# Kernel optimization log

Hardware: AMD Instinct MI355X
Metric: run time of the kernel (lower is better)

The kernel has to match this reference:

```python
import jax, jax.numpy as jnp
import numpy as np

B, T, D, H = 4, 1024, 1024, 16
TP = 1024
HD = D // H
LN_EPS = 1e-3  # keras LayerNormalization default epsilon


def snac_linear(x, wt, mt):
    # conv1dsnac: w = tanh(wt) * sigmoid(mt), shape [1, nx, nf] -> [nx, nf]
    w = (jnp.tanh(wt) * jax.nn.sigmoid(mt))[0]
    return jnp.einsum('btx,xf->btf', x, w)


def layernorm(x, gamma, beta):
    mu = jnp.mean(x, axis=-1, keepdims=True)
    var = jnp.mean(jnp.square(x - mu), axis=-1, keepdims=True)
    return (x - mu) * jax.lax.rsqrt(var + LN_EPS) * gamma + beta


def setup_inputs() -> dict:
    key = jax.random.key(0)
    ks = jax.random.split(key, 10)
    s = 0.02
    return {
        'input': jax.random.normal(ks[0], (B, T, D), jnp.float32),
        'past': jax.random.normal(ks[1], (B, 2, H, TP, HD), jnp.float32),
        'qkv_wt': jax.random.normal(ks[2], (1, D, 3 * D), jnp.float32) * s,
        'qkv_mt': jax.random.normal(ks[3], (1, D, 3 * D), jnp.float32) * s,
        'merge_wt': jax.random.normal(ks[4], (1, D, D), jnp.float32) * s,
        'merge_mt': jax.random.normal(ks[5], (1, D, D), jnp.float32) * s,
        'ln1_wt': jax.random.normal(ks[6], (1, D, D), jnp.float32) * s,
        'ln1_mt': jax.random.normal(ks[7], (1, D, D), jnp.float32) * s,
        'g1': jnp.ones((D,), jnp.float32), 'b1': jnp.zeros((D,), jnp.float32),
        'g2': jnp.ones((D,), jnp.float32), 'b2': jnp.zeros((D,), jnp.float32),
    }


def reference(input, past, qkv_wt, qkv_mt, merge_wt, merge_mt, ln1_wt, ln1_mt, g1, b1, g2, b2):
    x = input
    xn = layernorm(x, g1, b1)
    c = snac_linear(xn, qkv_wt, qkv_mt)  # [B, T, 3D]
    q, k, v = jnp.split(c, 3, axis=2)
    # split heads -> [B, H, T, HD]
    to_heads = lambda t: t.reshape(B, T, H, HD).transpose(0, 2, 1, 3)
    q, k, v = to_heads(q), to_heads(k), to_heads(v)
    present = jnp.stack([k, v], axis=1)  # [B, 2, H, T, HD]
    pk, pv = past[:, 0], past[:, 1]
    k = jnp.concatenate([pk, k], axis=2)  # [B, H, TP+T, HD]
    v = jnp.concatenate([pv, v], axis=2)
    nd, ns = T, TP + T
    w = jnp.einsum('bhqd,bhkd->bhqk', q, k) * jax.lax.rsqrt(jnp.float32(HD))
    i = jnp.arange(nd)[:, None]
    j = jnp.arange(ns)[None, :]
    m = (i >= j - ns + nd).astype(w.dtype)  # [nd, ns] causal mask incl. past
    w = w * m - jnp.asarray(1e10, w.dtype) * (1 - m)
    msk = jax.nn.softmax(w, axis=-1)  # [B, H, T, TP+T]
    a = jnp.einsum('bhqk,bhkd->bhqd', msk, v)
    ah = a.transpose(0, 2, 1, 3).reshape(B, T, D)  # merge heads
    am = snac_linear(ah, merge_wt, merge_mt)
    xa = x + am
    mlp = snac_linear(layernorm(xa, g2, b2), ln1_wt, ln1_mt)
    xm = xa + mlp
    return xm, present, msk
```

## Files before the change

kernel.cpp:

```cpp
#include <hip/hip_runtime.h>
#include <hip/hip_bf16.h>

typedef _Float16 half8 __attribute__((ext_vector_type(8)));
typedef _Float16 half4v __attribute__((ext_vector_type(4)));
typedef float f32x4 __attribute__((ext_vector_type(4)));

#define DEV static __device__ __forceinline__


typedef __attribute__((address_space(1))) const unsigned int* gas_p;
typedef __attribute__((address_space(3))) unsigned int* las_p;
DEV void glds16(const void* g, void* s) {
  __builtin_amdgcn_global_load_lds((gas_p)g, (las_p)s, 16, 0, 0);
}

__global__ __launch_bounds__(256) void prep_all(const float* __restrict__ qkv_wt,
                                                const float* __restrict__ qkv_mt,
                                                const float* __restrict__ mg_wt,
                                                const float* __restrict__ mg_mt,
                                                const float* __restrict__ l1_wt,
                                                const float* __restrict__ l1_mt,
                                                _Float16* __restrict__ wq,
                                                _Float16* __restrict__ wm,
                                                _Float16* __restrict__ wl) {
  __shared__ float tile[64][65];
  const float *wt, *mt;
  _Float16* out;
  int N, bid;
  if (blockIdx.x < 768) {
    wt = qkv_wt; mt = qkv_mt; out = wq; N = 3072; bid = blockIdx.x;
  } else if (blockIdx.x < 1024) {
    wt = mg_wt; mt = mg_mt; out = wm; N = 1024; bid = blockIdx.x - 768;
  } else {
    wt = l1_wt; mt = l1_mt; out = wl; N = 1024; bid = blockIdx.x - 1024;
  }
  const int ntiles = N >> 6;
  const int nt = bid % ntiles, kt = bid / ntiles;
  const int k0 = kt << 6, n0 = nt << 6;
  const int t = threadIdx.x, r = t >> 2, c0 = (t & 3) << 4;
  const long ibase = (long)(k0 + r) * N + n0 + c0;
#pragma unroll
  for (int j = 0; j < 16; j += 4) {
    float4 a = *(const float4*)(wt + ibase + j);
    float4 b = *(const float4*)(mt + ibase + j);
    tile[r][c0 + j + 0] = tanhf(a.x) / (1.f + __expf(-b.x));
    tile[r][c0 + j + 1] = tanhf(a.y) / (1.f + __expf(-b.y));
    tile[r][c0 + j + 2] = tanhf(a.z) / (1.f + __expf(-b.z));
    tile[r][c0 + j + 3] = tanhf(a.w) / (1.f + __expf(-b.w));
  }
  __syncthreads();
  half8 o0, o1;
#pragma unroll
  for (int j = 0; j < 8; ++j) {
    o0[j] = (_Float16)tile[c0 + j][r];
    o1[j] = (_Float16)tile[c0 + 8 + j][r];
  }
  _Float16* dst = out + (long)(n0 + r) * 1024 + k0 + c0;
  *(half8*)dst = o0;
  *(half8*)(dst + 8) = o1;
}

__global__ __launch_bounds__(256) void kv_prep(const float* __restrict__ past,
                                               const _Float16* __restrict__ vnew,
                                               _Float16* __restrict__ kf,
                                               _Float16* __restrict__ vt) {
  __shared__ float tile[64][65];
  if (blockIdx.x < 4096) {
    const long e = ((long)blockIdx.x * 256 + threadIdx.x) * 4;
    const int b = (int)(e >> 20);
    const int rem = (int)(e & 1048575);
    float4 v = *(const float4*)(past + (long)b * 2097152 + rem);
    half4v o = {(_Float16)v.x, (_Float16)v.y, (_Float16)v.z, (_Float16)v.w};
    const int h = rem >> 16, td = rem & 65535;
    *(half4v*)(kf + (long)(b * 16 + h) * 131072 + td) = o;
    return;
  }
  const int bid = blockIdx.x - 4096;
  const int bh = bid >> 5, kt = bid & 31;
  const int b = bh >> 4, h = bh & 15;
  const int k0 = kt << 6;
  const int t = threadIdx.x, r = t >> 2, c0 = (t & 3) << 4;
  if (k0 < 1024) {
    const float* src = past + (((long)(b * 2 + 1) * 16 + h) * 1024 + (k0 + r)) * 64 + c0;
#pragma unroll
    for (int j = 0; j < 16; j += 4) {
      float4 v = *(const float4*)(src + j);
      tile[r][c0 + j + 0] = v.x;
      tile[r][c0 + j + 1] = v.y;
      tile[r][c0 + j + 2] = v.z;
      tile[r][c0 + j + 3] = v.w;
    }
  } else {
    const _Float16* src = vnew + ((long)bh * 1024 + (k0 - 1024 + r)) * 64 + c0;
    half8 a = *(const half8*)src;
    half8 bq = *(const half8*)(src + 8);
#pragma unroll
    for (int j = 0; j < 8; ++j) {
      tile[r][c0 + j] = (float)a[j];
      tile[r][c0 + 8 + j] = (float)bq[j];
    }
  }
  __syncthreads();
  half8 o0, o1;
#pragma unroll
  for (int j = 0; j < 8; ++j) {
    o0[j] = (_Float16)tile[c0 + j][r];
    o1[j] = (_Float16)tile[c0 + 8 + j][r];
  }
  _Float16* dst = vt + ((long)bh * 64 + r) * 2048 + k0 + c0;
  *(half8*)dst = o0;
  *(half8*)(dst + 8) = o1;
}

template <int F16IN>
__global__ __launch_bounds__(256) void ln_k(const void* __restrict__ xin,
                                            const float* __restrict__ g,
                                            const float* __restrict__ be,
                                            _Float16* __restrict__ out) {
  __shared__ float red[4];
  const int row = blockIdx.x, tid = threadIdx.x, l = tid & 63, w = tid >> 6;
  float v0, v1, v2, v3;
  if constexpr (F16IN == 0) {
    float4 v = *(const float4*)((const float*)xin + (long)row * 1024 + tid * 4);
    v0 = v.x; v1 = v.y; v2 = v.z; v3 = v.w;
  } else {
    half4v v = *(const half4v*)((const _Float16*)xin + (long)row * 1024 + tid * 4);
    v0 = (float)v[0]; v1 = (float)v[1]; v2 = (float)v[2]; v3 = (float)v[3];
  }
  float s = v0 + v1 + v2 + v3;
#pragma unroll
  for (int o = 32; o > 0; o >>= 1) s += __shfl_down(s, o, 64);
  if (l == 0) red[w] = s;
  __syncthreads();
  const float mu = (red[0] + red[1] + red[2] + red[3]) * (1.f / 1024.f);
  float dx = v0 - mu, dy = v1 - mu, dz = v2 - mu, dw = v3 - mu;
  float ss = dx * dx + dy * dy + dz * dz + dw * dw;
#pragma unroll
  for (int o = 32; o > 0; o >>= 1) ss += __shfl_down(ss, o, 64);
  __syncthreads();
  if (l == 0) red[w] = ss;
  __syncthreads();
  const float var = (red[0] + red[1] + red[2] + red[3]) * (1.f / 1024.f);
  const float rs = rsqrtf(var + 1e-3f);
  float4 gv = *(const float4*)(g + tid * 4);
  float4 bv = *(const float4*)(be + tid * 4);
  half4v o = {(_Float16)(dx * rs * gv.x + bv.x), (_Float16)(dy * rs * gv.y + bv.y),
              (_Float16)(dz * rs * gv.z + bv.z), (_Float16)(dw * rs * gv.w + bv.w)};
  *(half4v*)(out + (long)row * 1024 + tid * 4) = o;
}

template <int BM, int BN, int EPI>
__global__ __launch_bounds__(256) void gemm_k(const _Float16* __restrict__ A,
                                              const _Float16* __restrict__ Bt,
                                              int mtiles,
                                              _Float16* __restrict__ e_q,
                                              _Float16* __restrict__ e_k,
                                              _Float16* __restrict__ e_v,
                                              float* __restrict__ e_present,
                                              const void* __restrict__ e_resv,
                                              void* __restrict__ e_outv) {
  constexpr int FM = BM / 32, FN = BN / 32;
  __shared__ __align__(16) char smem[BM * 128 + BN * 128];
  char* As = smem;
  char* Bs = smem + BM * 128;
  const int tid = threadIdx.x, l = tid & 63, w = tid >> 6;
  const int wm = w >> 1, wn = w & 1;
  const int bm = blockIdx.x % mtiles, bn = blockIdx.x / mtiles;
  const long m0 = (long)bm * BM, n0 = (long)bn * BN;

  f32x4 acc[FM][FN];
#pragma unroll
  for (int i = 0; i < FM; ++i)
#pragma unroll
    for (int j = 0; j < FN; ++j) acc[i][j] = (f32x4){0.f, 0.f, 0.f, 0.f};

  for (int kt = 0; kt < 16; ++kt) {
#pragma unroll
    for (int i = 0; i < FM; ++i) {
      const int cid = i * 256 + tid, row = cid >> 3, u = cid & 7;
      glds16(A + (m0 + row) * 1024 + kt * 64 + ((u ^ (row & 7)) << 3),
             As + i * 4096 + w * 1024);
    }
#pragma unroll
    for (int i = 0; i < FN; ++i) {
      const int cid = i * 256 + tid, row = cid >> 3, u = cid & 7;
      glds16(Bt + (n0 + row) * 1024 + kt * 64 + ((u ^ (row & 7)) << 3),
             Bs + i * 4096 + w * 1024);
    }
    __syncthreads();
    __builtin_amdgcn_s_setprio(1);
#pragma unroll
    for (int k2 = 0; k2 < 2; ++k2) {
      const int sl = k2 * 4 + (l >> 4);
      half8 bfr[FN];
#pragma unroll
      for (int fn = 0; fn < FN; ++fn) {
        const int rn = wn * (BN / 2) + fn * 16 + (l & 15);
        bfr[fn] = *(const half8*)(Bs + rn * 128 + ((sl ^ (rn & 7)) << 4));
      }
#pragma unroll
      for (int fm = 0; fm < FM; ++fm) {
        const int rm = wm * (BM / 2) + fm * 16 + (l & 15);
        const half8 afr = *(const half8*)(As + rm * 128 + ((sl ^ (rm & 7)) << 4));
#pragma unroll
        for (int fn = 0; fn < FN; ++fn)
          acc[fm][fn] = __builtin_amdgcn_mfma_f32_16x16x32_f16(afr, bfr[fn], acc[fm][fn], 0, 0, 0);
      }
    }
    __builtin_amdgcn_s_setprio(0);
    __syncthreads();
  }
#pragma unroll
  for (int fm = 0; fm < FM; ++fm) {
#pragma unroll
    for (int fn = 0; fn < FN; ++fn) {
#pragma unroll
      for (int r = 0; r < 4; ++r) {
        const long row = m0 + wm * (BM / 2) + fm * 16 + (l >> 4) * 4 + r;
        const long col = n0 + wn * (BN / 2) + fn * 16 + (l & 15);
        const float v = acc[fm][fn][r];
        if constexpr (EPI == 0) {
          const int b = (int)(row >> 10), t = (int)(row & 1023);
          const int sec = (int)(col >> 10), h = ((int)col >> 6) & 15, hd = (int)col & 63;
          const long bh = b * 16 + h;
          if (sec == 0) {
            e_q[(bh * 1024 + t) * 64 + hd] = (_Float16)v;
          } else if (sec == 1) {
            e_present[(((long)(b * 2) * 16 + h) * 1024 + t) * 64 + hd] = v;
            e_k[(bh * 2048 + 1024 + t) * 64 + hd] = (_Float16)v;
          } else {
            e_present[(((long)(b * 2 + 1) * 16 + h) * 1024 + t) * 64 + hd] = v;
            e_v[(bh * 1024 + t) * 64 + hd] = (_Float16)v;
          }
        } else if constexpr (EPI == 1) {
          ((_Float16*)e_outv)[row * 1024 + col] =
              (_Float16)(((const float*)e_resv)[row * 1024 + col] + v);
        } else {
          ((float*)e_outv)[row * 1024 + col] =
              (float)((const _Float16*)e_resv)[row * 1024 + col] + v;
        }
      }
    }
  }
}

__global__ __launch_bounds__(256, 4) void attn_k(const _Float16* __restrict__ qg,
                                                 const _Float16* __restrict__ kg,
                                                 const _Float16* __restrict__ vtg,
                                                 float* __restrict__ msk,
                                                 _Float16* __restrict__ ah) {
  __shared__ __align__(16) char smem[40960];
  char* ps_all = smem + 32768;
  const int tid = threadIdx.x, l = tid & 63, w = tid >> 6;
  char* psw = ps_all + w * 2048;
  const int lq = l & 15, hi = l >> 4;

  const int x = blockIdx.x & 7, g = blockIdx.x >> 3;
  const int bh = (g & 7) * 8 + x;
  const int qt = 15 - (g >> 3);
  const int r0 = qt << 6;
  const int rowg0 = r0 + w * 16;

  const _Float16* kb = kg + (long)bh * 131072;
  const _Float16* vb = vtg + (long)bh * 131072;
  float* mskb = msk + ((long)bh * 1024 + rowg0) * 2048;

  half8 qa[2];
  {
    const _Float16* qp = qg + ((long)bh * 1024 + rowg0 + lq) * 64 + hi * 8;
    qa[0] = *(const half8*)qp;
    qa[1] = *(const half8*)(qp + 32);
  }

  constexpr float C1 = 0.125f * 1.44269504088896341f;
  const int lim = rowg0 + lq + 1024;

  const int nc1 = (r0 + 1215) >> 7;
  auto stageK128 = [&](int b, int c) {
#pragma unroll
    for (int i = 0; i < 4; ++i) {
      const int cid = i * 256 + tid, row = cid >> 3, u = cid & 7;
      glds16(kb + (long)(c * 128 + row) * 64 + ((u ^ (row & 7)) << 3),
             smem + b * 16384 + i * 4096 + w * 1024);
    }
  };
  float rsum = 0.f;
  stageK128(0, 0);
  __syncthreads();
  for (int c = 0; c < nc1; ++c) {
    const int cur = c & 1;
    if (c + 1 < nc1) stageK128(cur ^ 1, c + 1);
    const char* ks = smem + cur * 16384;
    f32x4 sa[8];
#pragma unroll
    for (int fn = 0; fn < 8; ++fn) sa[fn] = (f32x4){0.f, 0.f, 0.f, 0.f};
    __builtin_amdgcn_s_setprio(1);
#pragma unroll
    for (int k2 = 0; k2 < 2; ++k2) {
      const int sl = k2 * 4 + hi;
      half8 ak[8];
#pragma unroll
      for (int fn = 0; fn < 8; ++fn) {
        const int rn = fn * 16 + lq;
        ak[fn] = *(const half8*)(ks + rn * 128 + ((sl ^ (rn & 7)) << 4));
      }
#pragma unroll
      for (int fn = 0; fn < 8; ++fn)
        sa[fn] = __builtin_amdgcn_mfma_f32_16x16x32_f16(ak[fn], qa[k2], sa[fn], 0, 0, 0);
    }
    __builtin_amdgcn_s_setprio(0);
    if (c < nc1 - 1) {
#pragma unroll
      for (int fn = 0; fn < 8; ++fn)
#pragma unroll
        for (int r = 0; r < 4; ++r) rsum += __builtin_amdgcn_exp2f(sa[fn][r] * C1);
    } else {
#pragma unroll
      for (int fn = 0; fn < 8; ++fn)
#pragma unroll
        for (int r = 0; r < 4; ++r) {
          const int col = c * 128 + fn * 16 + hi * 4 + r;
          const float e = __builtin_amdgcn_exp2f(sa[fn][r] * C1);
          rsum += (col <= lim) ? e : 0.f;
        }
    }
    __syncthreads();
  }
  rsum += __shfl_xor(rsum, 16, 64);
  rsum += __shfl_xor(rsum, 32, 64);
  const float c2s = -__builtin_amdgcn_logf(rsum);

  const int nc = (r0 + 1151) >> 6;
  auto stageK = [&](int b, int c) {
#pragma unroll
    for (int i = 0; i < 2; ++i) {
      const int cid = i * 256 + tid, row = cid >> 3, u = cid & 7;
      glds16(kb + (long)(c * 64 + row) * 64 + ((u ^ (row & 7)) << 3),
             smem + b * 8192 + i * 4096 + w * 1024);
    }
  };
  auto stageV = [&](int b, int c) {
#pragma unroll
    for (int i = 0; i < 2; ++i) {
      const int cid = i * 256 + tid, row = cid >> 3, u = cid & 7;
      glds16(vb + (long)row * 2048 + c * 64 + ((u ^ (row & 7)) << 3),
             smem + 16384 + b * 8192 + i * 4096 + w * 1024);
    }
  };

  f32x4 pv[4];
#pragma unroll
  for (int j = 0; j < 4; ++j) pv[j] = (f32x4){0.f, 0.f, 0.f, 0.f};
  __syncthreads();
  stageK(0, 0);
  stageV(0, 0);
  __syncthreads();
  for (int c = 0; c < nc; ++c) {
    const int cur = c & 1;
    if (c + 1 < nc) {
      stageK(cur ^ 1, c + 1);
      stageV(cur ^ 1, c + 1);
    }
    const char* ks = smem + cur * 8192;
    f32x4 sa[4];
#pragma unroll
    for (int fn = 0; fn < 4; ++fn) sa[fn] = (f32x4){0.f, 0.f, 0.f, 0.f};
    __builtin_amdgcn_s_setprio(1);
#pragma unroll
    for (int k2 = 0; k2 < 2; ++k2) {
      const int sl = k2 * 4 + hi;
      half8 ak[4];
#pragma unroll
      for (int fn = 0; fn < 4; ++fn) {
        const int rn = fn * 16 + lq;
        ak[fn] = *(const half8*)(ks + rn * 128 + ((sl ^ (rn & 7)) << 4));
      }
#pragma unroll
      for (int fn = 0; fn < 4; ++fn)
        sa[fn] = __builtin_amdgcn_mfma_f32_16x16x32_f16(ak[fn], qa[k2], sa[fn], 0, 0, 0);
    }
    __builtin_amdgcn_s_setprio(0);
    const bool bound = (c == nc - 1);
#pragma unroll
    for (int fn = 0; fn < 4; ++fn) {
      float pr[4];
#pragma unroll
      for (int r = 0; r < 4; ++r) {
        float p = __builtin_amdgcn_exp2f(sa[fn][r] * C1 + c2s);
        if (bound) {
          const int col = c * 64 + fn * 16 + hi * 4 + r;
          p = (col <= lim) ? p : 0.f;
        }
        pr[r] = p;
      }
      *(float4*)(mskb + (long)lq * 2048 + c * 64 + fn * 16 + hi * 4) =
          make_float4(pr[0], pr[1], pr[2], pr[3]);
      const half4v hv = {(_Float16)pr[0], (_Float16)pr[1], (_Float16)pr[2],
                         (_Float16)pr[3]};
      const int bc = fn * 32 + hi * 8;
      *(half4v*)(psw + lq * 128 + ((((bc >> 4) ^ (lq & 7)) << 4) | (bc & 15))) = hv;
    }
    __builtin_amdgcn_wave_barrier();
    asm volatile("s_waitcnt lgkmcnt(0)" ::: "memory");
    __builtin_amdgcn_sched_barrier(0);
    const char* vs = smem + 16384 + cur * 8192;
    __builtin_amdgcn_s_setprio(1);
#pragma unroll
    for (int k2p = 0; k2p < 2; ++k2p) {
      const int sl2 = k2p * 4 + hi;
      const half8 pa = *(const half8*)(psw + lq * 128 + ((sl2 ^ (lq & 7)) << 4));
      half8 bv[4];
#pragma unroll
      for (int fn2 = 0; fn2 < 4; ++fn2) {
        const int rd = fn2 * 16 + lq;
        bv[fn2] = *(const half8*)(vs + rd * 128 + ((sl2 ^ (rd & 7)) << 4));
      }
#pragma unroll
      for (int fn2 = 0; fn2 < 4; ++fn2)
        pv[fn2] = __builtin_amdgcn_mfma_f32_16x16x32_f16(pa, bv[fn2], pv[fn2], 0, 0, 0);
    }
    __builtin_amdgcn_s_setprio(0);
    __syncthreads();
  }

  const int ntail = 512 - (nc << 4);
  if (ntail > 0) {
    const float4 z4 = make_float4(0.f, 0.f, 0.f, 0.f);
    for (int row = 0; row < 16; ++row)
      for (int i = l; i < ntail; i += 64)
        *(float4*)(mskb + (long)row * 2048 + nc * 64 + i * 4) = z4;
  }

  const int b_ = bh >> 4, h_ = bh & 15;
  _Float16* ahb = ah + ((long)b_ * 1024 + rowg0) * 1024 + h_ * 64;
#pragma unroll
  for (int fn2 = 0; fn2 < 4; ++fn2)
#pragma unroll
    for (int r = 0; r < 4; ++r)
      ahb[(long)(hi * 4 + r) * 1024 + fn2 * 16 + lq] = (_Float16)pv[fn2][r];
}

extern "C" void kernel_launch(void* const* d_in, const int* in_sizes, int n_in,
                              void* d_out, int out_size, void* d_ws, size_t ws_size,
                              hipStream_t stream) {
  const float* x = (const float*)d_in[0];
  const float* past = (const float*)d_in[1];
  const float* qkv_wt = (const float*)d_in[2];
  const float* qkv_mt = (const float*)d_in[3];
  const float* merge_wt = (const float*)d_in[4];
  const float* merge_mt = (const float*)d_in[5];
  const float* ln1_wt = (const float*)d_in[6];
  const float* ln1_mt = (const float*)d_in[7];
  const float* g1 = (const float*)d_in[8];
  const float* b1 = (const float*)d_in[9];
  const float* g2 = (const float*)d_in[10];
  const float* b2 = (const float*)d_in[11];

  float* out = (float*)d_out;
  float* o_xm = out;
  float* o_present = out + 4194304;
  float* o_msk = out + 4194304 + 8388608;

  char* ws = (char*)d_ws;
  _Float16* wq_t = (_Float16*)(ws + 0);
  _Float16* wm_t = (_Float16*)(ws + 6291456);
  _Float16* wl_t = (_Float16*)(ws + 8388608);
  _Float16* xn   = (_Float16*)(ws + 10485760);
  _Float16* qws  = (_Float16*)(ws + 18874368);
  _Float16* kful = (_Float16*)(ws + 27262976);
  _Float16* vnew = (_Float16*)(ws + 44040192);
  _Float16* vt   = (_Float16*)(ws + 52428800);
  _Float16* ah   = (_Float16*)(ws + 69206016);
  _Float16* xa   = (_Float16*)(ws + 77594624);

  prep_all<<<1280, 256, 0, stream>>>(qkv_wt, qkv_mt, merge_wt, merge_mt, ln1_wt,
                                     ln1_mt, wq_t, wm_t, wl_t);
  ln_k<0><<<4096, 256, 0, stream>>>(x, g1, b1, xn);
  gemm_k<128, 128, 0><<<768, 256, 0, stream>>>(xn, wq_t, 32, qws, kful, vnew,
                                               o_present, nullptr, nullptr);
  kv_prep<<<6144, 256, 0, stream>>>(past, vnew, kful, vt);
  attn_k<<<1024, 256, 0, stream>>>(qws, kful, vt, o_msk, ah);
  gemm_k<64, 64, 1><<<1024, 256, 0, stream>>>(ah, wm_t, 64, nullptr, nullptr,
                                              nullptr, nullptr, x, xa);
  ln_k<1><<<4096, 256, 0, stream>>>(xa, g2, b2, xn);
  gemm_k<64, 64, 2><<<1024, 256, 0, stream>>>(xn, wl_t, 64, nullptr, nullptr,
                                              nullptr, nullptr, xa, o_xm);
}
```

Before: 315.6 us.

## Double-buffer GEMM LDS tiles, pass attention probabilities via shuffles, widen GEMM N-tile

The GEMM kernel now keeps two LDS buffers and loads the next K-tile while the MFMAs run on the current one, which removes the load-then-sync stall on every iteration. The attention kernel no longer writes the fp16 softmax probabilities to LDS and reads them back. It packs them with cvt_pkrtz and moves them into the A-operand layout with cross-lane shuffles, which drops 8 KB of LDS per block. The merge and MLP GEMMs switch to 64x128 tiles with half as many blocks. The cost is a larger LDS footprint in the GEMMs and round-toward-zero fp16 packing, which changes rounding slightly.

```diff
diff --git a/kernel.cpp b/kernel.cpp
--- a/kernel.cpp
+++ b/kernel.cpp
@@ -3,6 +3,7 @@
 
 typedef _Float16 half8 __attribute__((ext_vector_type(8)));
 typedef _Float16 half4v __attribute__((ext_vector_type(4)));
+typedef __fp16 fp16x2 __attribute__((ext_vector_type(2)));
 typedef float f32x4 __attribute__((ext_vector_type(4)));
 
 #define DEV static __device__ __forceinline__
@@ -12,6 +13,11 @@
 typedef __attribute__((address_space(3))) unsigned int* las_p;
 DEV void glds16(const void* g, void* s) {
   __builtin_amdgcn_global_load_lds((gas_p)g, (las_p)s, 16, 0, 0);
+}
+DEV unsigned int pk16(float a, float b) {
+  union { fp16x2 h; unsigned int u; } cv;
+  cv.h = __builtin_amdgcn_cvt_pkrtz(a, b);
+  return cv.u;
 }
 
 __global__ __launch_bounds__(256) void prep_all(const float* __restrict__ qkv_wt,
@@ -160,9 +166,8 @@
                                               const void* __restrict__ e_resv,
                                               void* __restrict__ e_outv) {
   constexpr int FM = BM / 32, FN = BN / 32;
-  __shared__ __align__(16) char smem[BM * 128 + BN * 128];
-  char* As = smem;
-  char* Bs = smem + BM * 128;
+  __shared__ __align__(16) char smem[2 * BM * 128 + 2 * BN * 128];
+  char* Bbase = smem + 2 * BM * 128;
   const int tid = threadIdx.x, l = tid & 63, w = tid >> 6;
   const int wm = w >> 1, wn = w & 1;
   const int bm = blockIdx.x % mtiles, bn = blockIdx.x / mtiles;
@@ -174,20 +179,28 @@
 #pragma unroll
     for (int j = 0; j < FN; ++j) acc[i][j] = (f32x4){0.f, 0.f, 0.f, 0.f};
 
-  for (int kt = 0; kt < 16; ++kt) {
+  auto stage = [&](int b, int kt) {
 #pragma unroll
     for (int i = 0; i < FM; ++i) {
       const int cid = i * 256 + tid, row = cid >> 3, u = cid & 7;
       glds16(A + (m0 + row) * 1024 + kt * 64 + ((u ^ (row & 7)) << 3),
-             As + i * 4096 + w * 1024);
+             smem + b * BM * 128 + i * 4096 + w * 1024);
     }
 #pragma unroll
     for (int i = 0; i < FN; ++i) {
       const int cid = i * 256 + tid, row = cid >> 3, u = cid & 7;
       glds16(Bt + (n0 + row) * 1024 + kt * 64 + ((u ^ (row & 7)) << 3),
-             Bs + i * 4096 + w * 1024);
-    }
-    __syncthreads();
+             Bbase + b * BN * 128 + i * 4096 + w * 1024);
+    }
+  };
+
+  stage(0, 0);
+  __syncthreads();
+  for (int kt = 0; kt < 16; ++kt) {
+    const int cur = kt & 1;
+    if (kt < 15) stage(cur ^ 1, kt + 1);
+    const char* As = smem + cur * BM * 128;
+    const char* Bs = Bbase + cur * BN * 128;
     __builtin_amdgcn_s_setprio(1);
 #pragma unroll
     for (int k2 = 0; k2 < 2; ++k2) {
@@ -249,10 +262,8 @@
                                                  const _Float16* __restrict__ vtg,
                                                  float* __restrict__ msk,
                                                  _Float16* __restrict__ ah) {
-  __shared__ __align__(16) char smem[40960];
-  char* ps_all = smem + 32768;
+  __shared__ __align__(16) char smem[32768];
   const int tid = threadIdx.x, l = tid & 63, w = tid >> 6;
-  char* psw = ps_all + w * 2048;
   const int lq = l & 15, hi = l >> 4;
 
   const int x = blockIdx.x & 7, g = blockIdx.x >> 3;
@@ -381,6 +392,7 @@
     }
     __builtin_amdgcn_s_setprio(0);
     const bool bound = (c == nc - 1);
+    unsigned int p32[8];
 #pragma unroll
     for (int fn = 0; fn < 4; ++fn) {
       float pr[4];
@@ -395,20 +407,22 @@
       }
       *(float4*)(mskb + (long)lq * 2048 + c * 64 + fn * 16 + hi * 4) =
           make_float4(pr[0], pr[1], pr[2], pr[3]);
-      const half4v hv = {(_Float16)pr[0], (_Float16)pr[1], (_Float16)pr[2],
-                         (_Float16)pr[3]};
-      const int bc = fn * 32 + hi * 8;
-      *(half4v*)(psw + lq * 128 + ((((bc >> 4) ^ (lq & 7)) << 4) | (bc & 15))) = hv;
-    }
-    __builtin_amdgcn_wave_barrier();
-    asm volatile("s_waitcnt lgkmcnt(0)" ::: "memory");
-    __builtin_amdgcn_sched_barrier(0);
+      p32[fn * 2] = pk16(pr[0], pr[1]);
+      p32[fn * 2 + 1] = pk16(pr[2], pr[3]);
+    }
     const char* vs = smem + 16384 + cur * 8192;
+    const int srcBase = lq + ((l & 16) << 1);
     __builtin_amdgcn_s_setprio(1);
 #pragma unroll
     for (int k2p = 0; k2p < 2; ++k2p) {
       const int sl2 = k2p * 4 + hi;
-      const half8 pa = *(const half8*)(psw + lq * 128 + ((sl2 ^ (lq & 7)) << 4));
+      union { unsigned int u[4]; half8 h; } pa;
+#pragma unroll
+      for (int j = 0; j < 4; ++j) {
+        const unsigned int word = (hi & 2) ? p32[4 * k2p + 2 + (j & 1)]
+                                           : p32[4 * k2p + (j & 1)];
+        pa.u[j] = __shfl((int)word, srcBase + ((j >> 1) << 4), 64);
+      }
       half8 bv[4];
 #pragma unroll
       for (int fn2 = 0; fn2 < 4; ++fn2) {
@@ -417,7 +431,7 @@
       }
 #pragma unroll
       for (int fn2 = 0; fn2 < 4; ++fn2)
-        pv[fn2] = __builtin_amdgcn_mfma_f32_16x16x32_f16(pa, bv[fn2], pv[fn2], 0, 0, 0);
+        pv[fn2] = __builtin_amdgcn_mfma_f32_16x16x32_f16(pa.h, bv[fn2], pv[fn2], 0, 0, 0);
     }
     __builtin_amdgcn_s_setprio(0);
     __syncthreads();
@@ -480,9 +494,9 @@
                                                o_present, nullptr, nullptr);
   kv_prep<<<6144, 256, 0, stream>>>(past, vnew, kful, vt);
   attn_k<<<1024, 256, 0, stream>>>(qws, kful, vt, o_msk, ah);
-  gemm_k<64, 64, 1><<<1024, 256, 0, stream>>>(ah, wm_t, 64, nullptr, nullptr,
+  gemm_k<64, 128, 1><<<512, 256, 0, stream>>>(ah, wm_t, 64, nullptr, nullptr,
                                               nullptr, nullptr, x, xa);
   ln_k<1><<<4096, 256, 0, stream>>>(xa, g2, b2, xn);
-  gemm_k<64, 64, 2><<<1024, 256, 0, stream>>>(xn, wl_t, 64, nullptr, nullptr,
+  gemm_k<64, 128, 2><<<512, 256, 0, stream>>>(xn, wl_t, 64, nullptr, nullptr,
                                               nullptr, nullptr, xa, o_xm);
 }
```

Measured after the change: 298.1 us. -5.5%, faster.
